# Kernel optimization log

Measured on AMD Instinct MI355X. Metric: run time of the kernel, lower is better.

Reference implementation:

```python
import jax, jax.numpy as jnp
import numpy as np


def _cft_icft_matrices(n):
    # Continuous FT over t in [0,1) sampled at n points, frequencies = fftfreq(n, d=1/n).
    # CFT  : X(f) = integral x(t) e^{-2pi i f t} dt  ~=  (1/n) * sum_t x(t) e^{-2pi i f t}
    # ICFT : x(t) = integral X(f) e^{+2pi i f t} df  ~=  df   * sum_f X(f) e^{+2pi i f t}
    # The original module evaluates the ICFT on the fftshift-ed frequency grid while the
    # coefficients stay in fft (unshifted) index order; we reproduce that pairing.
    sr = float(n)
    t = jnp.arange(n, dtype=jnp.float32) / n                      # [n]
    f = jnp.fft.fftfreq(n, d=1.0 / sr).astype(jnp.float32)        # [n], fft order
    f_shift = jnp.fft.fftshift(f)                                 # [n], shifted order
    two_pi = jnp.float32(2.0 * np.pi)
    dt = jnp.float32(1.0 / n)
    df = jnp.float32(sr / n)  # frequency spacing = 1.0 for unit duration
    # E_cft: [n_freq, n_time], E_icft: [n_time, n_freq]
    E_cft = jnp.exp(-1j * two_pi * f[:, None] * t[None, :]).astype(jnp.complex64) * dt
    E_icft = jnp.exp(1j * two_pi * t[:, None] * f_shift[None, :]).astype(jnp.complex64) * df
    return E_cft, E_icft


def setup_inputs() -> dict:
    key = jax.random.key(0)
    k1, k2, k3 = jax.random.split(key, 3)
    B, Ci, Co, n, modes = 32, 64, 64, 4096, 64
    scale = 1.0 / (Ci * Co)
    x = jax.random.normal(k1, (B, Ci, n), dtype=jnp.float32)
    # weights1 = scale * rand(Ci, Co, modes, cfloat): uniform[0,1) real and imag parts
    w_real = scale * jax.random.uniform(k2, (Ci, Co, modes), dtype=jnp.float32)
    w_imag = scale * jax.random.uniform(k3, (Ci, Co, modes), dtype=jnp.float32)
    return {"x": x, "w_real": w_real, "w_imag": w_imag}


def reference(x, w_real, w_imag):
    B, Ci, n = x.shape
    Co, modes = w_real.shape[1], w_real.shape[2]
    E_cft, E_icft = _cft_icft_matrices(n)
    w = (w_real + 1j * w_imag).astype(jnp.complex64)              # [Ci, Co, modes]
    xc = x.astype(jnp.complex64)
    # Batched CFT over all (batch, channel) pairs as one complex GEMM.
    x_cft = jnp.einsum('bit,ft->bif', xc, E_cft)                  # [B, Ci, n]
    # Spectral linear transform on the lowest `modes` frequencies.
    low = jnp.einsum('bif,iof->bof', x_cft[:, :, :modes], w)      # [B, Co, modes]
    out_ft = jnp.zeros((B, Co, n), dtype=jnp.complex64).at[:, :, :modes].set(low)
    # Batched ICFT back to the time grid; module returns the real part.
    out = jnp.einsum('bof,tf->bot', out_ft, E_icft)               # [B, Co, n]
    return out.real
```

## Files before the change

### kernel.cpp

```cpp
#include <hip/hip_runtime.h>
#include <math.h>

#define NT 4096
#define MODES 64
#define ROWS 2048
#define TWO_PI 6.283185307179586f
#define PI_F 3.14159265358979f

static __device__ __forceinline__ void rotm(float& wr, float& wi, float sr, float si) {
  float nr = fmaf(wr, sr, -wi * si);
  float ni = fmaf(wr, si,  wi * sr);
  wr = nr; wi = ni;
}

__global__ __launch_bounds__(256) void cft_fused_kernel(
    const float* __restrict__ x, float2* __restrict__ xfp,
    const float* __restrict__ w_real, const float* __restrict__ w_imag,
    float* __restrict__ wrt, float* __restrict__ wit, int S) {
  __shared__ __align__(16) char smem[33280];
  const int tid = threadIdx.x;
  const int nCft = 64 * S;

  if ((int)blockIdx.x >= nCft) {
    float (*tile)[65] = (float (*)[65])smem;
    const int bx = (int)blockIdx.x - nCft;
    const int sel = bx >> 6;
    const int io0 = (bx & 63) * 64;
    const float* __restrict__ src = sel ? w_imag : w_real;
    float* __restrict__ dst = sel ? wit : wrt;
#pragma unroll
    for (int j = 0; j < 4; ++j) {
      const int idx = tid + j * 256;
      const int r = idx >> 4;
      const int kq = idx & 15;
      float4 v = ((const float4*)src)[(size_t)(io0 + r) * 16 + kq];
      tile[r][4 * kq + 0] = v.x; tile[r][4 * kq + 1] = v.y;
      tile[r][4 * kq + 2] = v.z; tile[r][4 * kq + 3] = v.w;
    }
    __syncthreads();
#pragma unroll
    for (int j = 0; j < 16; ++j) {
      const int idx = tid + j * 256;
      const int k = idx >> 6;
      const int r = idx & 63;
      dst[(size_t)k * 4096 + io0 + r] = tile[r][k];
    }
    return;
  }

  float4* xs4 = (float4*)smem;
  const float* xsf = (const float*)smem;
  const int k0 = tid & 15;
  const int rg = tid >> 4;
  const int C = 512 / S;
  const int rowblk = (int)blockIdx.x / S;
  const int ts = (int)blockIdx.x % S;
  const int row0 = rowblk * 32;

  const int c4 = k0 & 3;
  const float p  = (c4 & 1) ? -1.f : 1.f;
  const float qc = (c4 == 0) ? 1.f : ((c4 == 2) ? -1.f : 0.f);
  const float rc = (c4 == 1) ? -1.f : ((c4 == 3) ? 1.f : 0.f);
  const int c8 = k0 & 7;
  float Aw, Bw;
  sincosf(-PI_F * (float)c8 * 0.25f, &Bw, &Aw);

  float st2r[4], st2i[4];
#pragma unroll
  for (int q = 0; q < 4; ++q) {
    const int k = k0 + 16 * q;
    sincosf(-TWO_PI * (float)(2 * k) / (float)NT, &st2i[q], &st2r[q]);
  }

  float ar[2][4] = {{0.f,0.f,0.f,0.f},{0.f,0.f,0.f,0.f}};
  float ai[2][4] = {{0.f,0.f,0.f,0.f},{0.f,0.f,0.f,0.f}};

  const float4* __restrict__ xg4 = (const float4*)x;
  const float2* bp0 = (const float2*)(xsf + (rg * 2 + 0) * 260);
  const float2* bp1 = (const float2*)(xsf + (rg * 2 + 1) * 260);

  for (int sub = 0; sub < C / 32; ++sub) {
    const int tl0 = ts * C + sub * 32;
    __syncthreads();
#pragma unroll
    for (int it = 0; it < 8; ++it) {
      const int idx = tid + it * 256;
      const int tlf = idx & 7;
      const int j = (idx >> 3) & 7;
      const int row = idx >> 6;
      xs4[row * 65 + j * 8 + tlf] =
          xg4[(size_t)(row0 + row) * (NT / 4) + j * 128 + (tl0 >> 2) + tlf];
    }
    __syncthreads();
    float wAr[4], wAi[4], wBr[4], wBi[4];
#pragma unroll
    for (int q = 0; q < 4; ++q) {
      const int k = k0 + 16 * q;
      const int phA = (k * tl0) & (NT - 1);
      const int phB = (k * (tl0 + 1)) & (NT - 1);
      sincosf(-TWO_PI * (float)phA / (float)NT, &wAi[q], &wAr[q]);
      sincosf(-TWO_PI * (float)phB / (float)NT, &wBi[q], &wBr[q]);
    }
#pragma unroll 2
    for (int tt = 0; tt < 16; ++tt) {
      float2 v0[8], v1[8];
#pragma unroll
      for (int j = 0; j < 8; ++j) {
        v0[j] = bp0[j * 16 + tt];
        v1[j] = bp1[j * 16 + tt];
      }
#pragma unroll
      for (int par = 0; par < 2; ++par) {
        const float* wrp = par ? wBr : wAr;
        const float* wip = par ? wBi : wAi;
#pragma unroll
        for (int rr = 0; rr < 2; ++rr) {
          const float2* v = rr ? v1 : v0;
          const float x0 = par ? v[0].y : v[0].x;
          const float x1 = par ? v[1].y : v[1].x;
          const float x2 = par ? v[2].y : v[2].x;
          const float x3 = par ? v[3].y : v[3].x;
          const float x4 = par ? v[4].y : v[4].x;
          const float x5 = par ? v[5].y : v[5].x;
          const float x6 = par ? v[6].y : v[6].x;
          const float x7 = par ? v[7].y : v[7].x;
          const float ue = fmaf(p, x4, x0), ve = fmaf(p, x6, x2);
          const float Er = fmaf(qc, ve, ue), Ei = rc * ve;
          const float uo = fmaf(p, x5, x1), vo = fmaf(p, x7, x3);
          const float Or_ = fmaf(qc, vo, uo), Oi_ = rc * vo;
          float sr = fmaf(Aw, Or_, Er); sr = fmaf(-Bw, Oi_, sr);
          float si = fmaf(Aw, Oi_, Ei); si = fmaf( Bw, Or_, si);
#pragma unroll
          for (int q = 0; q < 4; ++q) {
            ar[rr][q] = fmaf(sr, wrp[q], ar[rr][q]);
            ar[rr][q] = fmaf(-si, wip[q], ar[rr][q]);
            ai[rr][q] = fmaf(sr, wip[q], ai[rr][q]);
            ai[rr][q] = fmaf(si, wrp[q], ai[rr][q]);
          }
        }
      }
#pragma unroll
      for (int q = 0; q < 4; ++q) {
        rotm(wAr[q], wAi[q], st2r[q], st2i[q]);
        rotm(wBr[q], wBi[q], st2r[q], st2i[q]);
      }
    }
  }
  const float dt = 1.0f / (float)NT;
  const size_t base = ((size_t)ts * 64 + rowblk) * 64;
#pragma unroll
  for (int rr = 0; rr < 2; ++rr) {
    const int rl = rg * 2 + rr;
#pragma unroll
    for (int q = 0; q < 4; ++q) {
      xfp[(base + k0 + 16 * q) * 32 + rl] =
          make_float2(ar[rr][q] * dt, ai[rr][q] * dt);
    }
  }
}

__global__ __launch_bounds__(256) void mix_kernel(
    const float* __restrict__ wrt, const float* __restrict__ wit,
    const float2* __restrict__ xfp, float2* __restrict__ yf_t, int S) {
  __shared__ float2 wsc[4096];
  __shared__ float2 xsh[256];
  const int k = blockIdx.x & 63;
  const int bq = blockIdx.x >> 6;
  const int tid = threadIdx.x;
#pragma unroll
  for (int j = 0; j < 4; ++j) {
    const int idx = tid + 256 * j;
    float4 vr = ((const float4*)(wrt + (size_t)k * 4096))[idx];
    float4 vi = ((const float4*)(wit + (size_t)k * 4096))[idx];
    wsc[4 * idx + 0] = make_float2(vr.x, vi.x);
    wsc[4 * idx + 1] = make_float2(vr.y, vi.y);
    wsc[4 * idx + 2] = make_float2(vr.z, vi.z);
    wsc[4 * idx + 3] = make_float2(vr.w, vi.w);
  }
  {
    const int R = bq * 256 + tid;
    const int rowblk = R >> 5;
    const int rl = R & 31;
    float2 acc = make_float2(0.f, 0.f);
    for (int s = 0; s < S; ++s) {
      float2 v = xfp[(((size_t)s * 64 + rowblk) * 64 + k) * 32 + rl];
      acc.x += v.x; acc.y += v.y;
    }
    xsh[tid] = acc;
  }
  __syncthreads();
  const int o = tid & 63;
  const int bl = tid >> 6;
  float accr = 0.f, acci = 0.f;
#pragma unroll 8
  for (int i = 0; i < 64; ++i) {
    const float2 xv = xsh[bl * 64 + i];
    const float2 w = wsc[i * 64 + o];
    accr = fmaf(xv.x, w.x, accr); accr = fmaf(-xv.y, w.y, accr);
    acci = fmaf(xv.x, w.y, acci); acci = fmaf( xv.y, w.x, acci);
  }
  yf_t[(size_t)k * ROWS + bq * 256 + bl * 64 + o] = make_float2(accr, acci);
}

__global__ __launch_bounds__(256) void icft_kernel(const float2* __restrict__ yf_t,
                                                   float* __restrict__ out) {
  __shared__ float2 ysh[4][66];
  const int rgrp = blockIdx.x >> 1;
  const int tc = blockIdx.x & 1;
  const int row0 = rgrp * 4;
  const int tid = threadIdx.x;
  {
    const int k = tid >> 2;
    const int r = tid & 3;
    ysh[r][k] = yf_t[(size_t)k * ROWS + row0 + r];
  }
  __syncthreads();
  const int tl = tc * 256 + tid;
  float stepr, stepi;
  sincosf(TWO_PI * (float)tl / (float)NT, &stepi, &stepr);
  float wr = 1.f, wi = 0.f;
  float Gr[8][4] = {{0.f}};
  float Gi[8][4] = {{0.f}};
  for (int m = 0; m < 8; ++m) {
#pragma unroll
    for (int cc = 0; cc < 8; ++cc) {
      const int k = 8 * m + cc;
#pragma unroll
      for (int r = 0; r < 4; ++r) {
        const float2 y = ysh[r][k];
        Gr[cc][r] = fmaf(y.x, wr, Gr[cc][r]);
        Gr[cc][r] = fmaf(-y.y, wi, Gr[cc][r]);
        if (cc != 0 && cc != 4) {
          Gi[cc][r] = fmaf(y.x, wi, Gi[cc][r]);
          Gi[cc][r] = fmaf(y.y, wr, Gi[cc][r]);
        }
      }
      rotm(wr, wi, stepr, stepi);
    }
  }
  const float KK = 0.7071067811865476f;
  const float sgn = (tl & 1) ? -1.f : 1.f;
#pragma unroll
  for (int r = 0; r < 4; ++r) {
    const float Ae = (Gr[0][r] + Gr[2][r]) + (Gr[4][r] + Gr[6][r]);
    const float Ao = (Gr[1][r] + Gr[3][r]) + (Gr[5][r] + Gr[7][r]);
    const float A2 = (Gr[0][r] - Gr[2][r]) + (Gr[4][r] - Gr[6][r]);
    const float B2 = (Gi[1][r] - Gi[3][r]) + (Gi[5][r] - Gi[7][r]);
    const float P  = Gr[0][r] - Gr[4][r];
    const float Qr = (Gr[1][r] - Gr[3][r]) - (Gr[5][r] - Gr[7][r]);
    const float R  = Gi[6][r] - Gi[2][r];
    const float Qi = (Gi[5][r] - Gi[1][r]) + (Gi[7][r] - Gi[3][r]);
    const float U = P + R, V = P - R;
    const float W1 = KK * (Qr + Qi), W2 = KK * (Qr - Qi);
    float* op = out + (size_t)(row0 + r) * NT + tl;
    op[0]    = sgn * (Ae + Ao);
    op[512]  = sgn * (U + W1);
    op[1024] = sgn * (A2 - B2);
    op[1536] = sgn * (V - W2);
    op[2048] = sgn * (Ae - Ao);
    op[2560] = sgn * (U - W1);
    op[3072] = sgn * (A2 + B2);
    op[3584] = sgn * (V + W2);
  }
}

extern "C" void kernel_launch(void* const* d_in, const int* in_sizes, int n_in,
                              void* d_out, int out_size, void* d_ws, size_t ws_size,
                              hipStream_t stream) {
  const float* x      = (const float*)d_in[0];
  const float* w_real = (const float*)d_in[1];
  const float* w_imag = (const float*)d_in[2];
  float* out = (float*)d_out;

  const size_t MB = (size_t)ROWS * MODES * sizeof(float2);
  int S = 16;
  while (S > 4 && (size_t)(S + 4) * MB > ws_size) S >>= 1;

  char* wsp = (char*)d_ws;
  float2* xfp  = (float2*)wsp;
  float2* yf_t = (float2*)(wsp + (size_t)S * MB);
  float*  wrt  = (float*)(wsp + (size_t)(S + 2) * MB);
  float*  wit  = (float*)(wsp + (size_t)(S + 3) * MB);

  cft_fused_kernel<<<64 * S + 128, 256, 0, stream>>>(x, xfp, w_real, w_imag,
                                                     wrt, wit, S);
  mix_kernel<<<512, 256, 0, stream>>>(wrt, wit, xfp, yf_t, S);
  icft_kernel<<<1024, 256, 0, stream>>>(yf_t, out);
}
```

Before: 49.66 us.

## Precompute CFT twiddles in shared memory and remap threads to 8 modes by 32 rows

The CFT stage now computes twiddle factors for each 16-sample sub-tile once per block into shared memory, instead of every thread keeping rotating twiddles in registers and applying complex rotations. The thread mapping also changes from 16 mode-groups by 2 rows per thread to 8 mode-groups by 1 row per thread with 8 accumulators per row. The x tile shrinks to 16 samples, which halves the work per sync and doubles the number of sync rounds. The aim is to cut per-thread sincos and rotation work and register pressure, at the cost of more shared-memory loads for twiddles and more barriers.

```diff
diff --git a/kernel.cpp b/kernel.cpp
--- a/kernel.cpp
+++ b/kernel.cpp
@@ -17,7 +17,7 @@
     const float* __restrict__ x, float2* __restrict__ xfp,
     const float* __restrict__ w_real, const float* __restrict__ w_imag,
     float* __restrict__ wrt, float* __restrict__ wit, int S) {
-  __shared__ __align__(16) char smem[33280];
+  __shared__ __align__(16) char smem[25344];
   const int tid = threadIdx.x;
   const int nCft = 64 * S;
 
@@ -48,10 +48,10 @@
     return;
   }
 
-  float4* xs4 = (float4*)smem;
-  const float* xsf = (const float*)smem;
-  const int k0 = tid & 15;
-  const int rg = tid >> 4;
+  float* xsf = (float*)smem;
+  float2* tws = (float2*)(smem + 16896);
+  const int k0 = tid & 7;
+  const int rg = tid >> 3;
   const int C = 512 / S;
   const int rowblk = (int)blockIdx.x / S;
   const int ts = (int)blockIdx.x % S;
@@ -61,101 +61,74 @@
   const float p  = (c4 & 1) ? -1.f : 1.f;
   const float qc = (c4 == 0) ? 1.f : ((c4 == 2) ? -1.f : 0.f);
   const float rc = (c4 == 1) ? -1.f : ((c4 == 3) ? 1.f : 0.f);
-  const int c8 = k0 & 7;
   float Aw, Bw;
-  sincosf(-PI_F * (float)c8 * 0.25f, &Bw, &Aw);
-
-  float st2r[4], st2i[4];
-#pragma unroll
-  for (int q = 0; q < 4; ++q) {
-    const int k = k0 + 16 * q;
-    sincosf(-TWO_PI * (float)(2 * k) / (float)NT, &st2i[q], &st2r[q]);
-  }
-
-  float ar[2][4] = {{0.f,0.f,0.f,0.f},{0.f,0.f,0.f,0.f}};
-  float ai[2][4] = {{0.f,0.f,0.f,0.f},{0.f,0.f,0.f,0.f}};
+  sincosf(-PI_F * (float)k0 * 0.25f, &Bw, &Aw);
+
+  float ar[8] = {0.f,0.f,0.f,0.f,0.f,0.f,0.f,0.f};
+  float ai[8] = {0.f,0.f,0.f,0.f,0.f,0.f,0.f,0.f};
 
   const float4* __restrict__ xg4 = (const float4*)x;
-  const float2* bp0 = (const float2*)(xsf + (rg * 2 + 0) * 260);
-  const float2* bp1 = (const float2*)(xsf + (rg * 2 + 1) * 260);
-
-  for (int sub = 0; sub < C / 32; ++sub) {
-    const int tl0 = ts * C + sub * 32;
+  const float2* bp = (const float2*)(xsf + rg * 132);
+
+  for (int sub = 0; sub < C / 16; ++sub) {
+    const int tl0 = ts * C + sub * 16;
     __syncthreads();
 #pragma unroll
-    for (int it = 0; it < 8; ++it) {
+    for (int it = 0; it < 4; ++it) {
       const int idx = tid + it * 256;
-      const int tlf = idx & 7;
-      const int j = (idx >> 3) & 7;
-      const int row = idx >> 6;
-      xs4[row * 65 + j * 8 + tlf] =
+      const int tlf = idx & 3;
+      const int j = (idx >> 2) & 7;
+      const int row = idx >> 5;
+      ((float4*)xsf)[row * 33 + j * 4 + tlf] =
           xg4[(size_t)(row0 + row) * (NT / 4) + j * 128 + (tl0 >> 2) + tlf];
     }
+#pragma unroll
+    for (int it = 0; it < 4; ++it) {
+      const int e = tid + it * 256;
+      const int tl = e >> 6;
+      const int k = e & 63;
+      const int ph = (k * (tl0 + tl)) & (NT - 1);
+      float swr, swi;
+      sincosf(-TWO_PI * (float)ph / (float)NT, &swi, &swr);
+      tws[tl * 66 + k] = make_float2(swr, swi);
+    }
     __syncthreads();
-    float wAr[4], wAi[4], wBr[4], wBi[4];
-#pragma unroll
-    for (int q = 0; q < 4; ++q) {
-      const int k = k0 + 16 * q;
-      const int phA = (k * tl0) & (NT - 1);
-      const int phB = (k * (tl0 + 1)) & (NT - 1);
-      sincosf(-TWO_PI * (float)phA / (float)NT, &wAi[q], &wAr[q]);
-      sincosf(-TWO_PI * (float)phB / (float)NT, &wBi[q], &wBr[q]);
-    }
 #pragma unroll 2
-    for (int tt = 0; tt < 16; ++tt) {
-      float2 v0[8], v1[8];
-#pragma unroll
-      for (int j = 0; j < 8; ++j) {
-        v0[j] = bp0[j * 16 + tt];
-        v1[j] = bp1[j * 16 + tt];
-      }
+    for (int tt = 0; tt < 8; ++tt) {
+      float2 v[8];
+#pragma unroll
+      for (int j = 0; j < 8; ++j) v[j] = bp[j * 8 + tt];
 #pragma unroll
       for (int par = 0; par < 2; ++par) {
-        const float* wrp = par ? wBr : wAr;
-        const float* wip = par ? wBi : wAi;
-#pragma unroll
-        for (int rr = 0; rr < 2; ++rr) {
-          const float2* v = rr ? v1 : v0;
-          const float x0 = par ? v[0].y : v[0].x;
-          const float x1 = par ? v[1].y : v[1].x;
-          const float x2 = par ? v[2].y : v[2].x;
-          const float x3 = par ? v[3].y : v[3].x;
-          const float x4 = par ? v[4].y : v[4].x;
-          const float x5 = par ? v[5].y : v[5].x;
-          const float x6 = par ? v[6].y : v[6].x;
-          const float x7 = par ? v[7].y : v[7].x;
-          const float ue = fmaf(p, x4, x0), ve = fmaf(p, x6, x2);
-          const float Er = fmaf(qc, ve, ue), Ei = rc * ve;
-          const float uo = fmaf(p, x5, x1), vo = fmaf(p, x7, x3);
-          const float Or_ = fmaf(qc, vo, uo), Oi_ = rc * vo;
-          float sr = fmaf(Aw, Or_, Er); sr = fmaf(-Bw, Oi_, sr);
-          float si = fmaf(Aw, Oi_, Ei); si = fmaf( Bw, Or_, si);
-#pragma unroll
-          for (int q = 0; q < 4; ++q) {
-            ar[rr][q] = fmaf(sr, wrp[q], ar[rr][q]);
-            ar[rr][q] = fmaf(-si, wip[q], ar[rr][q]);
-            ai[rr][q] = fmaf(sr, wip[q], ai[rr][q]);
-            ai[rr][q] = fmaf(si, wrp[q], ai[rr][q]);
-          }
+        const int tl = 2 * tt + par;
+        const float x0 = par ? v[0].y : v[0].x;
+        const float x1 = par ? v[1].y : v[1].x;
+        const float x2 = par ? v[2].y : v[2].x;
+        const float x3 = par ? v[3].y : v[3].x;
+        const float x4 = par ? v[4].y : v[4].x;
+        const float x5 = par ? v[5].y : v[5].x;
+        const float x6 = par ? v[6].y : v[6].x;
+        const float x7 = par ? v[7].y : v[7].x;
+        const float ue = fmaf(p, x4, x0), ve = fmaf(p, x6, x2);
+        const float Er = fmaf(qc, ve, ue), Ei = rc * ve;
+        const float uo = fmaf(p, x5, x1), vo = fmaf(p, x7, x3);
+        const float Or_ = fmaf(qc, vo, uo), Oi_ = rc * vo;
+        float sr = fmaf(Aw, Or_, Er); sr = fmaf(-Bw, Oi_, sr);
+        float si = fmaf(Aw, Oi_, Ei); si = fmaf( Bw, Or_, si);
+#pragma unroll
+        for (int q = 0; q < 8; ++q) {
+          const float2 w = tws[tl * 66 + k0 + 8 * q];
+          ar[q] = fmaf(sr, w.x, ar[q]); ar[q] = fmaf(-si, w.y, ar[q]);
+          ai[q] = fmaf(sr, w.y, ai[q]); ai[q] = fmaf( si, w.x, ai[q]);
         }
       }
-#pragma unroll
-      for (int q = 0; q < 4; ++q) {
-        rotm(wAr[q], wAi[q], st2r[q], st2i[q]);
-        rotm(wBr[q], wBi[q], st2r[q], st2i[q]);
-      }
     }
   }
   const float dt = 1.0f / (float)NT;
   const size_t base = ((size_t)ts * 64 + rowblk) * 64;
 #pragma unroll
-  for (int rr = 0; rr < 2; ++rr) {
-    const int rl = rg * 2 + rr;
-#pragma unroll
-    for (int q = 0; q < 4; ++q) {
-      xfp[(base + k0 + 16 * q) * 32 + rl] =
-          make_float2(ar[rr][q] * dt, ai[rr][q] * dt);
-    }
+  for (int q = 0; q < 8; ++q) {
+    xfp[(base + k0 + 8 * q) * 32 + rg] = make_float2(ar[q] * dt, ai[q] * dt);
   }
 }
 
```

Result: faster. 47.63 us (-4.1%).
